# Kernel tuning notes

Hardware: AMD Instinct MI355X
Metric: run time of the kernel (lower is better)

Reference implementation:

```python
import jax, jax.numpy as jnp
import numpy as np

B, NV, NQ = 32, 256, 512
VD, QD, HD, K, HOUT = 512, 512, 512, 3, 8
HK = HD * K
BN_EPS = 1e-5


def _wn_linear(x, V, g, b):
    # weight_norm with dim=None: w = g * V / ||V||_F (scalar g)
    w = V * (g / jnp.linalg.norm(V))
    return x @ w.T + b


def setup_inputs() -> dict:
    key = jax.random.key(0)
    ks = jax.random.split(key, 12)
    n = lambda i, shape, s=1.0: jax.random.normal(ks[i], shape, jnp.float32) * s
    return {
        "v": n(0, (B, NV, VD)),
        "q": n(1, (B, NQ, QD)),
        # v_net / q_net: single weight-normed Linear + ReLU (dropout is eval-identity)
        "v_V": n(2, (HK, VD), 0.02),
        "v_g": jnp.float32(12.0),
        "v_b": n(3, (HK,), 0.02),
        "q_V": n(4, (HK, QD), 0.02),
        "q_g": jnp.float32(12.0),
        "q_b": n(5, (HK,), 0.02),
        "h_mat": n(6, (1, HOUT, 1, HK)),
        "h_bias": n(7, (1, HOUT, 1, 1)),
        "bn_gamma": jnp.ones((HD,), jnp.float32),
        "bn_beta": jnp.zeros((HD,), jnp.float32),
    }


def reference(v, q, v_V, v_g, v_b, q_V, q_g, q_b, h_mat, h_bias, bn_gamma, bn_beta):
    # projected features: (B, NV, HK) and (B, NQ, HK)
    v_ = jax.nn.relu(_wn_linear(v, v_V, v_g, v_b))
    q_ = jax.nn.relu(_wn_linear(q, q_V, q_g, q_b))
    # bilinear attention maps: (B, HOUT, NV, NQ)
    att_maps = jnp.einsum('hk,bvk,bqk->bhvq', h_mat[0, :, 0, :], v_, q_) + h_bias
    # fused version of the per-head loop: sum over heads h of einsum('bvk,bvq,bqk->bk')
    fusion = jnp.einsum('bvk,bhvq,bqk->bk', v_, att_maps, q_)  # (B, HK)
    # AvgPool1d(k, stride=k) * k == sum over contiguous groups of k
    logits = fusion.reshape(B, HD, K).sum(-1)
    # BatchNorm1d with batch statistics (train-mode math, biased variance)
    mu = logits.mean(axis=0)
    var = jnp.mean((logits - mu) ** 2, axis=0)
    logits = (logits - mu) * jax.lax.rsqrt(var + BN_EPS) * bn_gamma + bn_beta
    return logits, att_maps
```

## Files before the change

kernel.cpp:

```cpp
#include <hip/hip_runtime.h>
#include <hip/hip_bf16.h>

typedef unsigned short u16;
typedef unsigned int   u32;

typedef __attribute__((ext_vector_type(8))) short bhalf8;
typedef __attribute__((ext_vector_type(4))) float floatx4;

#define DEVI __device__ __forceinline__

DEVI float b2f(u16 x) { return __uint_as_float(((u32)x) << 16); }
DEVI u16 f2b(float f) {
    u32 u = __float_as_uint(f);
    u32 r = u + 0x7fffu + ((u >> 16) & 1u);
    return (u16)(r >> 16);
}
DEVI u32 pack2(float lo, float hi) {
    __hip_bfloat162 t = __float22bfloat162_rn(float2{lo, hi});
    union { __hip_bfloat162 b; u32 u; } c; c.b = t; return c.u;
}
DEVI u32 bmul2f(u32 a, u32 h) {
    float al = __uint_as_float(a << 16);
    float ah = __uint_as_float(a & 0xffff0000u);
    float hl = __uint_as_float(h << 16);
    float hh = __uint_as_float(h & 0xffff0000u);
    return pack2(al * hl, ah * hh);
}

DEVI void async16(const void* g, void* l) {
    __builtin_amdgcn_global_load_lds(
        (const __attribute__((address_space(1))) u32*)g,
        (__attribute__((address_space(3))) u32*)l, 16, 0, 0);
}

DEVI uint4 ld8(const void* p, size_t ei, int f32) {
    if (f32) {
        const float* f = (const float*)p + ei;
        float4 a = *(const float4*)f;
        float4 b = *(const float4*)(f + 4);
        uint4 r;
        r.x = pack2(a.x, a.y);
        r.y = pack2(a.z, a.w);
        r.z = pack2(b.x, b.y);
        r.w = pack2(b.z, b.w);
        return r;
    }
    return *(const uint4*)((const u16*)p + ei);
}
DEVI float ld1(const void* p, size_t ei, int f32) {
    return f32 ? ((const float*)p)[ei] : b2f(((const u16*)p)[ei]);
}
DEVI void st1(void* p, size_t ei, float v, int f32) {
    if (f32) ((float*)p)[ei] = v;
    else     ((u16*)p)[ei] = f2b(v);
}

__global__ void detect_kernel(const u32* __restrict__ bng, const u32* __restrict__ vg,
                              int* __restrict__ flags) {
    if (threadIdx.x == 0 && blockIdx.x == 0) {
        flags[0] = (bng[0] == 0x3F800000u) ? 1 : 0;
        flags[1] = (vg[0]  == 0x41400000u) ? 1 : 0;
    }
}

__global__ void convert_kernel(const void* __restrict__ src, u16* __restrict__ dst,
                               int n8, float* __restrict__ ssq,
                               const int* __restrict__ flags) {
    const int fa = flags[0];
    int i = blockIdx.x * 256 + threadIdx.x;
    const int stride = gridDim.x * 256;
    float s = 0.f;
    for (int c = i; c < n8; c += stride) {
        uint4 x = ld8(src, (size_t)c * 8, fa);
        *(uint4*)(dst + (size_t)c * 8) = x;
        if (ssq) {
            u32 a[4] = {x.x, x.y, x.z, x.w};
#pragma unroll
            for (int j = 0; j < 4; ++j) {
                float l = b2f((u16)a[j]), h = b2f((u16)(a[j] >> 16));
                s += l * l + h * h;
            }
        }
    }
    if (ssq) {
#pragma unroll
        for (int off = 32; off; off >>= 1) s += __shfl_down(s, off);
        if ((threadIdx.x & 63) == 0) atomicAdd(ssq, s);
    }
}

__global__ void sumsq_kernel(const void* __restrict__ a, const void* __restrict__ b,
                             float* __restrict__ out, const int* __restrict__ flags) {
    const int fa = flags[0];
    const int tid = threadIdx.x;
    int gid = blockIdx.x * 256 + tid;
    const int stride = gridDim.x * 256;
    float s0 = 0.f, s1 = 0.f;
    for (int c = gid; c < 786432 / 8; c += stride) {
        uint4 x = ld8(a, (size_t)c * 8, fa);
        uint4 y = ld8(b, (size_t)c * 8, fa);
        u32 ax[4] = {x.x, x.y, x.z, x.w};
        u32 ay[4] = {y.x, y.y, y.z, y.w};
#pragma unroll
        for (int i = 0; i < 4; ++i) {
            float l0 = b2f((u16)ax[i]), h0 = b2f((u16)(ax[i] >> 16));
            s0 += l0 * l0 + h0 * h0;
            float l1 = b2f((u16)ay[i]), h1 = b2f((u16)(ay[i] >> 16));
            s1 += l1 * l1 + h1 * h1;
        }
    }
#pragma unroll
    for (int off = 32; off; off >>= 1) {
        s0 += __shfl_down(s0, off);
        s1 += __shfl_down(s1, off);
    }
    if ((tid & 63) == 0) { atomicAdd(&out[0], s0); atomicAdd(&out[1], s1); }
}

DEVI bhalf8 fragLd(const u16* T, int row, int kb) {
    return *(const bhalf8*)&T[(row * 8 + (kb ^ (row & 7))) * 8];
}

__global__ __launch_bounds__(256, 2)
void proj_fast(const u16* __restrict__ X, const u16* __restrict__ V,
               const void* __restrict__ bias, const void* __restrict__ g,
               const float* __restrict__ sumsq, int sumsqIdx,
               u16* __restrict__ out, const int* __restrict__ flags) {
    const int fa = flags[0], fs = flags[1];
    const int tid = threadIdx.x, lane = tid & 63, w = tid >> 6;
    const int quad = lane >> 4, l15 = lane & 15;
    const int mBase = blockIdx.y * 128, nBase = blockIdx.x * 128;
    const int moff = (w & 1) * 64, noff = (w >> 1) * 64;
    __shared__ __align__(16) u16 As[128 * 64];
    __shared__ __align__(16) u16 Bs[128 * 64];
    floatx4 acc[4][4];
#pragma unroll
    for (int mi = 0; mi < 4; ++mi)
#pragma unroll
        for (int ni = 0; ni < 4; ++ni) acc[mi][ni] = floatx4{0.f, 0.f, 0.f, 0.f};

    for (int k0 = 0; k0 < 512; k0 += 64) {
#pragma unroll
        for (int r = 0; r < 4; ++r) {
            int s = r * 256 + tid;
            int row = s >> 3;
            int kb = (s & 7) ^ (row & 7);
            async16(X + (size_t)(mBase + row) * 512 + k0 + kb * 8,
                    As + (size_t)(r * 256 + w * 64) * 8);
            async16(V + (size_t)(nBase + row) * 512 + k0 + kb * 8,
                    Bs + (size_t)(r * 256 + w * 64) * 8);
        }
        __syncthreads();
#pragma unroll
        for (int ks = 0; ks < 64; ks += 32) {
            bhalf8 af[4], bfr[4];
#pragma unroll
            for (int i = 0; i < 4; ++i)
                af[i] = fragLd(As, moff + i * 16 + l15, (ks >> 3) + quad);
#pragma unroll
            for (int i = 0; i < 4; ++i)
                bfr[i] = fragLd(Bs, noff + i * 16 + l15, (ks >> 3) + quad);
#pragma unroll
            for (int mi = 0; mi < 4; ++mi)
#pragma unroll
                for (int ni = 0; ni < 4; ++ni)
                    acc[mi][ni] = __builtin_amdgcn_mfma_f32_16x16x32_bf16(
                        af[mi], bfr[ni], acc[mi][ni], 0, 0, 0);
        }
        __syncthreads();
    }
    const float scale = ld1(g, 0, fs) / sqrtf(sumsq[sumsqIdx]);
#pragma unroll
    for (int ni = 0; ni < 4; ++ni) {
        const int col = nBase + noff + ni * 16 + l15;
        const float bv = ld1(bias, col, fa);
#pragma unroll
        for (int mi = 0; mi < 4; ++mi) {
            const int rowb = mBase + moff + mi * 16 + quad * 4;
#pragma unroll
            for (int r = 0; r < 4; ++r) {
                float vv = acc[mi][ni][r] * scale + bv;
                vv = vv > 0.f ? vv : 0.f;
                out[(size_t)(rowb + r) * 1536 + col] = f2b(vv);
            }
        }
    }
}

__global__ __launch_bounds__(256, 2)
void proj_slow(const void* __restrict__ X, const void* __restrict__ V,
               const void* __restrict__ bias, const void* __restrict__ g,
               const float* __restrict__ sumsq, int sumsqIdx,
               u16* __restrict__ out, const int* __restrict__ flags) {
    const int fa = flags[0], fs = flags[1];
    const int tid = threadIdx.x, lane = tid & 63, w = tid >> 6;
    const int quad = lane >> 4, l15 = lane & 15;
    const int mBase = blockIdx.y * 128, nBase = blockIdx.x * 128;
    const int moff = (w & 1) * 64, noff = (w >> 1) * 64;
    __shared__ __align__(16) u16 As[128 * 64];
    __shared__ __align__(16) u16 Bs[128 * 64];
    floatx4 acc[4][4];
#pragma unroll
    for (int mi = 0; mi < 4; ++mi)
#pragma unroll
        for (int ni = 0; ni < 4; ++ni) acc[mi][ni] = floatx4{0.f, 0.f, 0.f, 0.f};

    for (int k0 = 0; k0 < 512; k0 += 64) {
        uint4 xa[4], xb[4];
#pragma unroll
        for (int r = 0; r < 4; ++r) {
            int s = r * 256 + tid;
            int row = s >> 3, kb = (s & 7) ^ (row & 7);
            xa[r] = ld8(X, (size_t)(mBase + row) * 512 + k0 + kb * 8, fa);
            xb[r] = ld8(V, (size_t)(nBase + row) * 512 + k0 + kb * 8, fa);
        }
#pragma unroll
        for (int r = 0; r < 4; ++r) {
            int s = r * 256 + tid;
            *(uint4*)&As[s * 8] = xa[r];
            *(uint4*)&Bs[s * 8] = xb[r];
        }
        __syncthreads();
#pragma unroll
        for (int ks = 0; ks < 64; ks += 32) {
            bhalf8 af[4], bfr[4];
#pragma unroll
            for (int i = 0; i < 4; ++i)
                af[i] = fragLd(As, moff + i * 16 + l15, (ks >> 3) + quad);
#pragma unroll
            for (int i = 0; i < 4; ++i)
                bfr[i] = fragLd(Bs, noff + i * 16 + l15, (ks >> 3) + quad);
#pragma unroll
            for (int mi = 0; mi < 4; ++mi)
#pragma unroll
                for (int ni = 0; ni < 4; ++ni)
                    acc[mi][ni] = __builtin_amdgcn_mfma_f32_16x16x32_bf16(
                        af[mi], bfr[ni], acc[mi][ni], 0, 0, 0);
        }
        __syncthreads();
    }
    const float scale = ld1(g, 0, fs) / sqrtf(sumsq[sumsqIdx]);
#pragma unroll
    for (int ni = 0; ni < 4; ++ni) {
        const int col = nBase + noff + ni * 16 + l15;
        const float bv = ld1(bias, col, fa);
#pragma unroll
        for (int mi = 0; mi < 4; ++mi) {
            const int rowb = mBase + moff + mi * 16 + quad * 4;
#pragma unroll
            for (int r = 0; r < 4; ++r) {
                float vv = acc[mi][ni][r] * scale + bv;
                vv = vv > 0.f ? vv : 0.f;
                out[(size_t)(rowb + r) * 1536 + col] = f2b(vv);
            }
        }
    }
}

__global__ __launch_bounds__(256, 2)
void att_kernel(const u16* __restrict__ v_, const u16* __restrict__ q_,
                const void* __restrict__ hmat, const void* __restrict__ hbias,
                void* __restrict__ dout, u16* __restrict__ sOut,
                const int* __restrict__ flags) {
    const int fa = flags[0];
    const int b = blockIdx.z, h = blockIdx.y;
    const int mt = blockIdx.x;
    const int tid = threadIdx.x, lane = tid & 63, w = tid >> 6;
    const int quad = lane >> 4, l15 = lane & 15;
    const int noff = w * 128;
    __shared__ __align__(16) u16 As[64 * 64];
    __shared__ __align__(16) u16 Bs[512 * 64];
    __shared__ __align__(16) u16 Hs[1536];
    const u16* vp = v_ + (size_t)b * 256 * 1536;
    const u16* qp = q_ + (size_t)b * 512 * 1536;

    if (h < 8) {
        if (tid < 192) *(uint4*)&Hs[tid * 8] = ld8(hmat, (size_t)h * 1536 + tid * 8, fa);
    } else {
        for (int k = tid; k < 1536; k += 256) {
            float s = 0.f;
#pragma unroll
            for (int hh = 0; hh < 8; ++hh) s += ld1(hmat, (size_t)hh * 1536 + k, fa);
            Hs[k] = f2b(s);
        }
    }
    __syncthreads();

    floatx4 acc[4][8];
#pragma unroll
    for (int mi = 0; mi < 4; ++mi)
#pragma unroll
        for (int ni = 0; ni < 8; ++ni) acc[mi][ni] = floatx4{0.f, 0.f, 0.f, 0.f};

    for (int k0 = 0; k0 < 1536; k0 += 64) {
#pragma unroll
        for (int r = 0; r < 16; ++r) {
            int s = r * 256 + tid;
            int row = s >> 3, kb = (s & 7) ^ (row & 7);
            async16(qp + (size_t)row * 1536 + k0 + kb * 8,
                    Bs + (size_t)(r * 256 + w * 64) * 8);
        }
#pragma unroll
        for (int r = 0; r < 2; ++r) {
            int s = r * 256 + tid;
            int row = s >> 3, kb = (s & 7) ^ (row & 7);
            uint4 a = *(const uint4*)(vp + (size_t)(mt * 64 + row) * 1536 + k0 + kb * 8);
            uint4 hh = *(const uint4*)&Hs[k0 + kb * 8];
            uint4 res;
            res.x = bmul2f(a.x, hh.x); res.y = bmul2f(a.y, hh.y);
            res.z = bmul2f(a.z, hh.z); res.w = bmul2f(a.w, hh.w);
            *(uint4*)&As[s * 8] = res;
        }
        __syncthreads();
#pragma unroll
        for (int ks = 0; ks < 64; ks += 32) {
            bhalf8 af[4], bfr[8];
#pragma unroll
            for (int i = 0; i < 4; ++i)
                af[i] = fragLd(As, i * 16 + l15, (ks >> 3) + quad);
#pragma unroll
            for (int i = 0; i < 8; ++i)
                bfr[i] = fragLd(Bs, noff + i * 16 + l15, (ks >> 3) + quad);
#pragma unroll
            for (int mi = 0; mi < 4; ++mi)
#pragma unroll
                for (int ni = 0; ni < 8; ++ni)
                    acc[mi][ni] = __builtin_amdgcn_mfma_f32_16x16x32_bf16(
                        af[mi], bfr[ni], acc[mi][ni], 0, 0, 0);
        }
        __syncthreads();
    }

    if (h < 8) {
        const float bias = ld1(hbias, h, fa);
        const size_t obase = 16384 + ((size_t)(b * 8 + h)) * 256 * 512;
#pragma unroll
        for (int mi = 0; mi < 4; ++mi) {
            const int vg = mt * 64 + mi * 16 + quad * 4;
#pragma unroll
            for (int ni = 0; ni < 8; ++ni) {
                const int qg = noff + ni * 16 + l15;
#pragma unroll
                for (int r = 0; r < 4; ++r)
                    st1(dout, obase + (size_t)(vg + r) * 512 + qg,
                        acc[mi][ni][r] + bias, fa);
            }
        }
    } else {
        float sbias = 0.f;
#pragma unroll
        for (int hh = 0; hh < 8; ++hh) sbias += ld1(hbias, hh, fa);
        u16* sp = sOut + (size_t)b * 256 * 512;
#pragma unroll
        for (int mi = 0; mi < 4; ++mi) {
            const int vg = mt * 64 + mi * 16 + quad * 4;
#pragma unroll
            for (int ni = 0; ni < 8; ++ni) {
                const int qg = noff + ni * 16 + l15;
#pragma unroll
                for (int r = 0; r < 4; ++r)
                    sp[(size_t)(vg + r) * 512 + qg] = f2b(acc[mi][ni][r] + sbias);
            }
        }
    }
}

__global__ __launch_bounds__(256, 2)
void fusion_kernel(const u16* __restrict__ s, const u16* __restrict__ q_,
                   const u16* __restrict__ v_, float* __restrict__ fusion) {
    const int b = blockIdx.y;
    const int vt = blockIdx.x / 12, kt = blockIdx.x % 12;
    const int tid = threadIdx.x, lane = tid & 63, w = tid >> 6;
    const int quad = lane >> 4, l15 = lane & 15;
    const int moff = (w & 1) * 64, noff = (w >> 1) * 64;
    __shared__ __align__(16) u16 As[128 * 64];
    __shared__ __align__(16) u16 Bs[128 * 64];
    const u16* ap = s + (size_t)b * 256 * 512;
    const u16* qp = q_ + (size_t)b * 512 * 1536;
    floatx4 acc[4][4];
#pragma unroll
    for (int mi = 0; mi < 4; ++mi)
#pragma unroll
        for (int ni = 0; ni < 4; ++ni) acc[mi][ni] = floatx4{0.f, 0.f, 0.f, 0.f};

    for (int q0 = 0; q0 < 512; q0 += 64) {
#pragma unroll
        for (int r = 0; r < 4; ++r) {
            int sl = r * 256 + tid;
            int row = sl >> 3, kb = (sl & 7) ^ (row & 7);
            async16(ap + (size_t)(vt * 128 + row) * 512 + q0 + kb * 8,
                    As + (size_t)(r * 256 + w * 64) * 8);
        }
        union { uint4 q4; u16 e[8]; } pk[4];
#pragma unroll
        for (int r = 0; r < 4; ++r) {
            int chunk = r * 256 + tid;
            int qq = chunk >> 4, n8 = chunk & 15;
            pk[r].q4 = *(const uint4*)(qp + (size_t)(q0 + qq) * 1536 + kt * 128 + n8 * 8);
        }
#pragma unroll
        for (int r = 0; r < 4; ++r) {
            int chunk = r * 256 + tid;
            int qq = chunk >> 4, n8 = chunk & 15;
            const int qs = qq ^ ((n8 & 7) << 3);
#pragma unroll
            for (int j = 0; j < 8; ++j)
                Bs[(n8 * 8 + j) * 64 + qs] = pk[r].e[j];
        }
        __syncthreads();
#pragma unroll
        for (int ks = 0; ks < 64; ks += 32) {
            bhalf8 af[4], bfr[4];
#pragma unroll
            for (int i = 0; i < 4; ++i)
                af[i] = fragLd(As, moff + i * 16 + l15, (ks >> 3) + quad);
#pragma unroll
            for (int i = 0; i < 4; ++i) {
                const int n = noff + i * 16 + l15;
                const int blk = ((ks >> 3) + quad) ^ ((n >> 3) & 7);
                bfr[i] = *(const bhalf8*)&Bs[n * 64 + (blk << 3)];
            }
#pragma unroll
            for (int mi = 0; mi < 4; ++mi)
#pragma unroll
                for (int ni = 0; ni < 4; ++ni)
                    acc[mi][ni] = __builtin_amdgcn_mfma_f32_16x16x32_bf16(
                        af[mi], bfr[ni], acc[mi][ni], 0, 0, 0);
        }
        __syncthreads();
    }
    const u16* vb = v_ + (size_t)b * 256 * 1536;
#pragma unroll
    for (int ni = 0; ni < 4; ++ni) {
        const int kg = kt * 128 + noff + ni * 16 + l15;
        float cs = 0.f;
#pragma unroll
        for (int mi = 0; mi < 4; ++mi) {
            const int vg = vt * 128 + moff + mi * 16 + quad * 4;
#pragma unroll
            for (int r = 0; r < 4; ++r)
                cs += acc[mi][ni][r] * b2f(vb[(size_t)(vg + r) * 1536 + kg]);
        }
        cs += __shfl_xor(cs, 16);
        cs += __shfl_xor(cs, 32);
        if (quad == 0) atomicAdd(&fusion[b * 1536 + kg], cs);
    }
}

__global__ void logits_kernel(const float* __restrict__ fusion, const void* __restrict__ gamma,
                              const void* __restrict__ beta, void* __restrict__ dout,
                              const int* __restrict__ flags) {
    const int fa = flags[0];
    const int d = blockIdx.x * 64 + threadIdx.x;
    float g[32];
    float mu = 0.f;
#pragma unroll
    for (int b = 0; b < 32; ++b) {
        const float* f = fusion + b * 1536 + d * 3;
        g[b] = f[0] + f[1] + f[2];
        mu += g[b];
    }
    mu *= (1.f / 32.f);
    float var = 0.f;
#pragma unroll
    for (int b = 0; b < 32; ++b) { float t = g[b] - mu; var += t * t; }
    var *= (1.f / 32.f);
    const float rs = rsqrtf(var + 1e-5f);
    const float ga = ld1(gamma, d, fa), be = ld1(beta, d, fa);
#pragma unroll
    for (int b = 0; b < 32; ++b)
        st1(dout, (size_t)b * 512 + d, (g[b] - mu) * rs * ga + be, fa);
}

extern "C" void kernel_launch(void* const* d_in, const int* in_sizes, int n_in,
                              void* d_out, int out_size, void* d_ws, size_t ws_size,
                              hipStream_t stream) {
    const void* v   = d_in[0];
    const void* q   = d_in[1];
    const void* vV  = d_in[2];
    const void* vg  = d_in[3];
    const void* vb  = d_in[4];
    const void* qV  = d_in[5];
    const void* qg  = d_in[6];
    const void* qb  = d_in[7];
    const void* hm  = d_in[8];
    const void* hb  = d_in[9];
    const void* bng = d_in[10];
    const void* bnb = d_in[11];

    char* ws = (char*)d_ws;
    float* sums   = (float*)ws;
    int*   flags  = (int*)(ws + 64);
    float* fusion = (float*)(ws + 256);

    const size_t NEED = 104006144;
    const bool fast = (ws_size >= NEED);

    hipMemsetAsync(sums, 0, 8, stream);
    hipMemsetAsync(fusion, 0, 32 * 1536 * 4, stream);
    detect_kernel<<<dim3(1), dim3(64), 0, stream>>>((const u32*)bng, (const u32*)vg, flags);

    if (fast) {
        u16* sbuf = (u16*)(ws + 197120);
        u16* vbf  = (u16*)(ws + 197120);
        u16* vVbf = (u16*)(ws + 8585728);
        u16* qVbf = (u16*)(ws + 10158592);
        u16* v_   = (u16*)(ws + 11731456);
        u16* q_   = (u16*)(ws + 36897280);
        u16* qbf  = (u16*)(ws + 87228928);

        convert_kernel<<<dim3(512), dim3(256), 0, stream>>>(v,  vbf,  524288, nullptr, flags);
        convert_kernel<<<dim3(1024), dim3(256), 0, stream>>>(q, qbf, 1048576, nullptr, flags);
        convert_kernel<<<dim3(128), dim3(256), 0, stream>>>(vV, vVbf, 98304, sums + 0, flags);
        convert_kernel<<<dim3(128), dim3(256), 0, stream>>>(qV, qVbf, 98304, sums + 1, flags);

        proj_fast<<<dim3(12, 64), dim3(256), 0, stream>>>(vbf, vVbf, vb, vg, sums, 0, v_, flags);
        proj_fast<<<dim3(12, 128), dim3(256), 0, stream>>>(qbf, qVbf, qb, qg, sums, 1, q_, flags);
        att_kernel<<<dim3(4, 9, 32), dim3(256), 0, stream>>>(v_, q_, hm, hb, d_out, sbuf, flags);
        fusion_kernel<<<dim3(24, 32), dim3(256), 0, stream>>>(sbuf, q_, v_, fusion);
    } else {
        u16* sbuf = (u16*)(ws + 197120);
        u16* v_   = (u16*)(ws + 8585728);
        u16* q_   = (u16*)(ws + 33751552);

        sumsq_kernel<<<dim3(128), dim3(256), 0, stream>>>(vV, qV, sums, flags);
        proj_slow<<<dim3(12, 64), dim3(256), 0, stream>>>(v, vV, vb, vg, sums, 0, v_, flags);
        proj_slow<<<dim3(12, 128), dim3(256), 0, stream>>>(q, qV, qb, qg, sums, 1, q_, flags);
        att_kernel<<<dim3(4, 9, 32), dim3(256), 0, stream>>>(v_, q_, hm, hb, d_out, sbuf, flags);
        fusion_kernel<<<dim3(24, 32), dim3(256), 0, stream>>>(sbuf, q_, v_, fusion);
    }
    logits_kernel<<<dim3(8), dim3(64), 0, stream>>>(fusion, bng, bnb, d_out, flags);
}
```

Before: 462.4 us.

## Compute all heads per attention tile with double-buffered fp16 MFMA

The attention kernel is restructured so each 512-thread block handles a 64x128 (v,q) tile for all 8 heads at once. It reuses the same v/q fragments across heads by scaling the v fragment with each head's row in registers, and forms the head-summed map from the per-head accumulators. This replaces the old 9-block-per-tile scheme that reloaded q_ for every head plus a separate summed-head pass. Loads are double-buffered with async global-to-LDS copies, blocks are remapped with a swizzled 1D grid, and intermediates switch from bf16 to fp16 MFMA. The fp16 switch risks overflow or precision differences, and 64 fp32 accumulators plus a larger LDS footprint may limit occupancy.

```diff
diff --git a/kernel.cpp b/kernel.cpp
--- a/kernel.cpp
+++ b/kernel.cpp
@@ -1,10 +1,11 @@
 #include <hip/hip_runtime.h>
 #include <hip/hip_bf16.h>
+#include <hip/hip_fp16.h>
 
 typedef unsigned short u16;
 typedef unsigned int   u32;
 
-typedef __attribute__((ext_vector_type(8))) short bhalf8;
+typedef __attribute__((ext_vector_type(8))) _Float16 half8;
 typedef __attribute__((ext_vector_type(4))) float floatx4;
 
 #define DEVI __device__ __forceinline__
@@ -15,16 +16,16 @@
     u32 r = u + 0x7fffu + ((u >> 16) & 1u);
     return (u16)(r >> 16);
 }
-DEVI u32 pack2(float lo, float hi) {
-    __hip_bfloat162 t = __float22bfloat162_rn(float2{lo, hi});
-    union { __hip_bfloat162 b; u32 u; } c; c.b = t; return c.u;
-}
-DEVI u32 bmul2f(u32 a, u32 h) {
-    float al = __uint_as_float(a << 16);
-    float ah = __uint_as_float(a & 0xffff0000u);
-    float hl = __uint_as_float(h << 16);
-    float hh = __uint_as_float(h & 0xffff0000u);
-    return pack2(al * hl, ah * hh);
+DEVI u16 f2h(float f) {
+    union { _Float16 h; u16 u; } c; c.h = (_Float16)f; return c.u;
+}
+DEVI float h2f(u16 x) {
+    union { u16 u; _Float16 h; } c; c.u = x; return (float)c.h;
+}
+DEVI u32 packh2(float lo, float hi) {
+    union { __half2 h; u32 u; } c;
+    c.h = __floats2half2_rn(lo, hi);
+    return c.u;
 }
 
 DEVI void async16(const void* g, void* l) {
@@ -33,19 +34,24 @@
         (__attribute__((address_space(3))) u32*)l, 16, 0, 0);
 }
 
-DEVI uint4 ld8(const void* p, size_t ei, int f32) {
+DEVI uint4 ld8h(const void* p, size_t ei, int f32) {
+    uint4 r;
     if (f32) {
         const float* f = (const float*)p + ei;
         float4 a = *(const float4*)f;
         float4 b = *(const float4*)(f + 4);
-        uint4 r;
-        r.x = pack2(a.x, a.y);
-        r.y = pack2(a.z, a.w);
-        r.z = pack2(b.x, b.y);
-        r.w = pack2(b.z, b.w);
-        return r;
-    }
-    return *(const uint4*)((const u16*)p + ei);
+        r.x = packh2(a.x, a.y);
+        r.y = packh2(a.z, a.w);
+        r.z = packh2(b.x, b.y);
+        r.w = packh2(b.z, b.w);
+    } else {
+        uint4 x = *(const uint4*)((const u16*)p + ei);
+        r.x = packh2(b2f((u16)x.x), b2f((u16)(x.x >> 16)));
+        r.y = packh2(b2f((u16)x.y), b2f((u16)(x.y >> 16)));
+        r.z = packh2(b2f((u16)x.z), b2f((u16)(x.z >> 16)));
+        r.w = packh2(b2f((u16)x.w), b2f((u16)(x.w >> 16)));
+    }
+    return r;
 }
 DEVI float ld1(const void* p, size_t ei, int f32) {
     return f32 ? ((const float*)p)[ei] : b2f(((const u16*)p)[ei]);
@@ -53,6 +59,10 @@
 DEVI void st1(void* p, size_t ei, float v, int f32) {
     if (f32) ((float*)p)[ei] = v;
     else     ((u16*)p)[ei] = f2b(v);
+}
+
+DEVI floatx4 mfma16(half8 a, half8 b, floatx4 c) {
+    return __builtin_amdgcn_mfma_f32_16x16x32_f16(a, b, c, 0, 0, 0);
 }
 
 __global__ void detect_kernel(const u32* __restrict__ bng, const u32* __restrict__ vg,
@@ -71,13 +81,13 @@
     const int stride = gridDim.x * 256;
     float s = 0.f;
     for (int c = i; c < n8; c += stride) {
-        uint4 x = ld8(src, (size_t)c * 8, fa);
+        uint4 x = ld8h(src, (size_t)c * 8, fa);
         *(uint4*)(dst + (size_t)c * 8) = x;
         if (ssq) {
             u32 a[4] = {x.x, x.y, x.z, x.w};
 #pragma unroll
             for (int j = 0; j < 4; ++j) {
-                float l = b2f((u16)a[j]), h = b2f((u16)(a[j] >> 16));
+                float l = h2f((u16)a[j]), h = h2f((u16)(a[j] >> 16));
                 s += l * l + h * h;
             }
         }
@@ -97,15 +107,15 @@
     const int stride = gridDim.x * 256;
     float s0 = 0.f, s1 = 0.f;
     for (int c = gid; c < 786432 / 8; c += stride) {
-        uint4 x = ld8(a, (size_t)c * 8, fa);
-        uint4 y = ld8(b, (size_t)c * 8, fa);
+        uint4 x = ld8h(a, (size_t)c * 8, fa);
+        uint4 y = ld8h(b, (size_t)c * 8, fa);
         u32 ax[4] = {x.x, x.y, x.z, x.w};
         u32 ay[4] = {y.x, y.y, y.z, y.w};
 #pragma unroll
         for (int i = 0; i < 4; ++i) {
-            float l0 = b2f((u16)ax[i]), h0 = b2f((u16)(ax[i] >> 16));
+            float l0 = h2f((u16)ax[i]), h0 = h2f((u16)(ax[i] >> 16));
             s0 += l0 * l0 + h0 * h0;
-            float l1 = b2f((u16)ay[i]), h1 = b2f((u16)(ay[i] >> 16));
+            float l1 = h2f((u16)ay[i]), h1 = h2f((u16)(ay[i] >> 16));
             s1 += l1 * l1 + h1 * h1;
         }
     }
@@ -117,8 +127,8 @@
     if ((tid & 63) == 0) { atomicAdd(&out[0], s0); atomicAdd(&out[1], s1); }
 }
 
-DEVI bhalf8 fragLd(const u16* T, int row, int kb) {
-    return *(const bhalf8*)&T[(row * 8 + (kb ^ (row & 7))) * 8];
+DEVI half8 fragLd(const u16* T, int row, int kb) {
+    return *(const half8*)&T[(row * 8 + (kb ^ (row & 7))) * 8];
 }
 
 __global__ __launch_bounds__(256, 2)
@@ -153,7 +163,7 @@
         __syncthreads();
 #pragma unroll
         for (int ks = 0; ks < 64; ks += 32) {
-            bhalf8 af[4], bfr[4];
+            half8 af[4], bfr[4];
 #pragma unroll
             for (int i = 0; i < 4; ++i)
                 af[i] = fragLd(As, moff + i * 16 + l15, (ks >> 3) + quad);
@@ -164,8 +174,7 @@
             for (int mi = 0; mi < 4; ++mi)
 #pragma unroll
                 for (int ni = 0; ni < 4; ++ni)
-                    acc[mi][ni] = __builtin_amdgcn_mfma_f32_16x16x32_bf16(
-                        af[mi], bfr[ni], acc[mi][ni], 0, 0, 0);
+                    acc[mi][ni] = mfma16(af[mi], bfr[ni], acc[mi][ni]);
         }
         __syncthreads();
     }
@@ -181,7 +190,7 @@
             for (int r = 0; r < 4; ++r) {
                 float vv = acc[mi][ni][r] * scale + bv;
                 vv = vv > 0.f ? vv : 0.f;
-                out[(size_t)(rowb + r) * 1536 + col] = f2b(vv);
+                out[(size_t)(rowb + r) * 1536 + col] = f2h(vv);
             }
         }
     }
@@ -211,8 +220,8 @@
         for (int r = 0; r < 4; ++r) {
             int s = r * 256 + tid;
             int row = s >> 3, kb = (s & 7) ^ (row & 7);
-            xa[r] = ld8(X, (size_t)(mBase + row) * 512 + k0 + kb * 8, fa);
-            xb[r] = ld8(V, (size_t)(nBase + row) * 512 + k0 + kb * 8, fa);
+            xa[r] = ld8h(X, (size_t)(mBase + row) * 512 + k0 + kb * 8, fa);
+            xb[r] = ld8h(V, (size_t)(nBase + row) * 512 + k0 + kb * 8, fa);
         }
 #pragma unroll
         for (int r = 0; r < 4; ++r) {
@@ -223,7 +232,7 @@
         __syncthreads();
 #pragma unroll
         for (int ks = 0; ks < 64; ks += 32) {
-            bhalf8 af[4], bfr[4];
+            half8 af[4], bfr[4];
 #pragma unroll
             for (int i = 0; i < 4; ++i)
                 af[i] = fragLd(As, moff + i * 16 + l15, (ks >> 3) + quad);
@@ -234,8 +243,7 @@
             for (int mi = 0; mi < 4; ++mi)
 #pragma unroll
                 for (int ni = 0; ni < 4; ++ni)
-                    acc[mi][ni] = __builtin_amdgcn_mfma_f32_16x16x32_bf16(
-                        af[mi], bfr[ni], acc[mi][ni], 0, 0, 0);
+                    acc[mi][ni] = mfma16(af[mi], bfr[ni], acc[mi][ni]);
         }
         __syncthreads();
     }
@@ -251,115 +259,127 @@
             for (int r = 0; r < 4; ++r) {
                 float vv = acc[mi][ni][r] * scale + bv;
                 vv = vv > 0.f ? vv : 0.f;
-                out[(size_t)(rowb + r) * 1536 + col] = f2b(vv);
-            }
-        }
-    }
-}
-
-__global__ __launch_bounds__(256, 2)
+                out[(size_t)(rowb + r) * 1536 + col] = f2h(vv);
+            }
+        }
+    }
+}
+
+__global__ __launch_bounds__(512, 2)
 void att_kernel(const u16* __restrict__ v_, const u16* __restrict__ q_,
                 const void* __restrict__ hmat, const void* __restrict__ hbias,
                 void* __restrict__ dout, u16* __restrict__ sOut,
                 const int* __restrict__ flags) {
     const int fa = flags[0];
-    const int b = blockIdx.z, h = blockIdx.y;
-    const int mt = blockIdx.x;
+    const int phys = blockIdx.x;
+    const int logical = (phys & 7) * 64 + (phys >> 3);
+    const int b = logical >> 4;
+    const int mt = (logical >> 2) & 3;
+    const int nt = logical & 3;
     const int tid = threadIdx.x, lane = tid & 63, w = tid >> 6;
     const int quad = lane >> 4, l15 = lane & 15;
-    const int noff = w * 128;
-    __shared__ __align__(16) u16 As[64 * 64];
-    __shared__ __align__(16) u16 Bs[512 * 64];
-    __shared__ __align__(16) u16 Hs[1536];
-    const u16* vp = v_ + (size_t)b * 256 * 1536;
-    const u16* qp = q_ + (size_t)b * 512 * 1536;
-
-    if (h < 8) {
-        if (tid < 192) *(uint4*)&Hs[tid * 8] = ld8(hmat, (size_t)h * 1536 + tid * 8, fa);
-    } else {
-        for (int k = tid; k < 1536; k += 256) {
-            float s = 0.f;
-#pragma unroll
-            for (int hh = 0; hh < 8; ++hh) s += ld1(hmat, (size_t)hh * 1536 + k, fa);
-            Hs[k] = f2b(s);
-        }
-    }
+    const int wr = (w >> 2) * 32;
+    const int wc = (w & 3) * 32;
+
+    __shared__ __align__(16) u16 Af[2][64 * 64];
+    __shared__ __align__(16) u16 Bf[2][128 * 64];
+    __shared__ __align__(16) u16 Hs[8 * 1536];
+
+    const u16* vp = v_ + (size_t)b * 256 * 1536 + (size_t)mt * 64 * 1536;
+    const u16* qp = q_ + (size_t)b * 512 * 1536 + (size_t)nt * 128 * 1536;
+
+#pragma unroll
+    for (int r = 0; r < 3; ++r) {
+        int slot = r * 512 + tid;
+        *(uint4*)&Hs[slot * 8] = ld8h(hmat, (size_t)slot * 8, fa);
+    }
+
+    auto STAGE = [&](int pbuf, int k0s) {
+        int s = tid;
+        int row = s >> 3, kb = (s & 7) ^ (row & 7);
+        async16(vp + (size_t)row * 1536 + k0s + kb * 8, &Af[pbuf][(w * 64) * 8]);
+#pragma unroll
+        for (int r = 0; r < 2; ++r) {
+            int s2 = r * 512 + tid;
+            int row2 = s2 >> 3, kb2 = (s2 & 7) ^ (row2 & 7);
+            async16(qp + (size_t)row2 * 1536 + k0s + kb2 * 8,
+                    &Bf[pbuf][(r * 512 + w * 64) * 8]);
+        }
+    };
+
+    STAGE(0, 0);
     __syncthreads();
 
-    floatx4 acc[4][8];
-#pragma unroll
-    for (int mi = 0; mi < 4; ++mi)
-#pragma unroll
-        for (int ni = 0; ni < 8; ++ni) acc[mi][ni] = floatx4{0.f, 0.f, 0.f, 0.f};
-
-    for (int k0 = 0; k0 < 1536; k0 += 64) {
-#pragma unroll
-        for (int r = 0; r < 16; ++r) {
-            int s = r * 256 + tid;
-            int row = s >> 3, kb = (s & 7) ^ (row & 7);
-            async16(qp + (size_t)row * 1536 + k0 + kb * 8,
-                    Bs + (size_t)(r * 256 + w * 64) * 8);
-        }
-#pragma unroll
-        for (int r = 0; r < 2; ++r) {
-            int s = r * 256 + tid;
-            int row = s >> 3, kb = (s & 7) ^ (row & 7);
-            uint4 a = *(const uint4*)(vp + (size_t)(mt * 64 + row) * 1536 + k0 + kb * 8);
-            uint4 hh = *(const uint4*)&Hs[k0 + kb * 8];
-            uint4 res;
-            res.x = bmul2f(a.x, hh.x); res.y = bmul2f(a.y, hh.y);
-            res.z = bmul2f(a.z, hh.z); res.w = bmul2f(a.w, hh.w);
-            *(uint4*)&As[s * 8] = res;
-        }
-        __syncthreads();
-#pragma unroll
-        for (int ks = 0; ks < 64; ks += 32) {
-            bhalf8 af[4], bfr[8];
-#pragma unroll
-            for (int i = 0; i < 4; ++i)
-                af[i] = fragLd(As, i * 16 + l15, (ks >> 3) + quad);
-#pragma unroll
-            for (int i = 0; i < 8; ++i)
-                bfr[i] = fragLd(Bs, noff + i * 16 + l15, (ks >> 3) + quad);
-#pragma unroll
-            for (int mi = 0; mi < 4; ++mi)
-#pragma unroll
-                for (int ni = 0; ni < 8; ++ni)
-                    acc[mi][ni] = __builtin_amdgcn_mfma_f32_16x16x32_bf16(
-                        af[mi], bfr[ni], acc[mi][ni], 0, 0, 0);
-        }
-        __syncthreads();
-    }
-
-    if (h < 8) {
-        const float bias = ld1(hbias, h, fa);
+    floatx4 acc[8][2][2];
+#pragma unroll
+    for (int h = 0; h < 8; ++h)
+#pragma unroll
+        for (int mi = 0; mi < 2; ++mi)
+#pragma unroll
+            for (int ni = 0; ni < 2; ++ni) acc[h][mi][ni] = floatx4{0.f, 0.f, 0.f, 0.f};
+
+    int pb = 0;
+    for (int kt = 0; kt < 24; ++kt) {
+        const int k0 = kt * 64;
+        if (kt < 23) STAGE(pb ^ 1, k0 + 64);
+        const u16* As = Af[pb];
+        const u16* Bs = Bf[pb];
+#pragma unroll
+        for (int ks = 0; ks < 2; ++ks) {
+            const int ch = ks * 4 + quad;
+            half8 av0 = fragLd(As, wr + l15, ch);
+            half8 av1 = fragLd(As, wr + 16 + l15, ch);
+            half8 bq0 = fragLd(Bs, wc + l15, ch);
+            half8 bq1 = fragLd(Bs, wc + 16 + l15, ch);
+#pragma unroll
+            for (int h = 0; h < 8; ++h) {
+                half8 hf = *(const half8*)&Hs[h * 1536 + k0 + ch * 8];
+                half8 a0 = av0 * hf;
+                half8 a1 = av1 * hf;
+                acc[h][0][0] = mfma16(a0, bq0, acc[h][0][0]);
+                acc[h][0][1] = mfma16(a0, bq1, acc[h][0][1]);
+                acc[h][1][0] = mfma16(a1, bq0, acc[h][1][0]);
+                acc[h][1][1] = mfma16(a1, bq1, acc[h][1][1]);
+            }
+        }
+        __syncthreads();
+        pb ^= 1;
+    }
+
+    float hb8[8];
+    float sbias = 0.f;
+#pragma unroll
+    for (int h = 0; h < 8; ++h) { hb8[h] = ld1(hbias, h, fa); sbias += hb8[h]; }
+
+#pragma unroll
+    for (int h = 0; h < 8; ++h) {
         const size_t obase = 16384 + ((size_t)(b * 8 + h)) * 256 * 512;
 #pragma unroll
-        for (int mi = 0; mi < 4; ++mi) {
-            const int vg = mt * 64 + mi * 16 + quad * 4;
-#pragma unroll
-            for (int ni = 0; ni < 8; ++ni) {
-                const int qg = noff + ni * 16 + l15;
+        for (int mi = 0; mi < 2; ++mi) {
+            const int vg = mt * 64 + wr + mi * 16 + quad * 4;
+#pragma unroll
+            for (int ni = 0; ni < 2; ++ni) {
+                const int qg = nt * 128 + wc + ni * 16 + l15;
 #pragma unroll
                 for (int r = 0; r < 4; ++r)
                     st1(dout, obase + (size_t)(vg + r) * 512 + qg,
-                        acc[mi][ni][r] + bias, fa);
-            }
-        }
-    } else {
-        float sbias = 0.f;
-#pragma unroll
-        for (int hh = 0; hh < 8; ++hh) sbias += ld1(hbias, hh, fa);
-        u16* sp = sOut + (size_t)b * 256 * 512;
-#pragma unroll
-        for (int mi = 0; mi < 4; ++mi) {
-            const int vg = mt * 64 + mi * 16 + quad * 4;
-#pragma unroll
-            for (int ni = 0; ni < 8; ++ni) {
-                const int qg = noff + ni * 16 + l15;
-#pragma unroll
-                for (int r = 0; r < 4; ++r)
-                    sp[(size_t)(vg + r) * 512 + qg] = f2b(acc[mi][ni][r] + sbias);
+                        acc[h][mi][ni][r] + hb8[h], fa);
+            }
+        }
+    }
+    u16* sp = sOut + (size_t)b * 256 * 512;
+#pragma unroll
+    for (int mi = 0; mi < 2; ++mi) {
+        const int vg = mt * 64 + wr + mi * 16 + quad * 4;
+#pragma unroll
+        for (int ni = 0; ni < 2; ++ni) {
+            const int qg = nt * 128 + wc + ni * 16 + l15;
+#pragma unroll
+            for (int r = 0; r < 4; ++r) {
+                float s = sbias;
+#pragma unroll
+                for (int h = 0; h < 8; ++h) s += acc[h][mi][ni][r];
+                sp[(size_t)(vg + r) * 512 + qg] = f2h(s);
             }
         }
     }
@@ -410,7 +430,7 @@
         __syncthreads();
 #pragma unroll
         for (int ks = 0; ks < 64; ks += 32) {
-            bhalf8 af[4], bfr[4];
+            half8 af[4], bfr[4];
 #pragma unroll
             for (int i = 0; i < 4; ++i)
                 af[i] = fragLd(As, moff + i * 16 + l15, (ks >> 3) + quad);
@@ -418,14 +438,13 @@
             for (int i = 0; i < 4; ++i) {
                 const int n = noff + i * 16 + l15;
                 const int blk = ((ks >> 3) + quad) ^ ((n >> 3) & 7);
-                bfr[i] = *(const bhalf8*)&Bs[n * 64 + (blk << 3)];
+                bfr[i] = *(const half8*)&Bs[n * 64 + (blk << 3)];
             }
 #pragma unroll
             for (int mi = 0; mi < 4; ++mi)
 #pragma unroll
                 for (int ni = 0; ni < 4; ++ni)
-                    acc[mi][ni] = __builtin_amdgcn_mfma_f32_16x16x32_bf16(
-                        af[mi], bfr[ni], acc[mi][ni], 0, 0, 0);
+                    acc[mi][ni] = mfma16(af[mi], bfr[ni], acc[mi][ni]);
         }
         __syncthreads();
     }
@@ -439,7 +458,7 @@
             const int vg = vt * 128 + moff + mi * 16 + quad * 4;
 #pragma unroll
             for (int r = 0; r < 4; ++r)
-                cs += acc[mi][ni][r] * b2f(vb[(size_t)(vg + r) * 1536 + kg]);
+                cs += acc[mi][ni][r] * h2f(vb[(size_t)(vg + r) * 1536 + kg]);
         }
         cs += __shfl_xor(cs, 16);
         cs += __shfl_xor(cs, 32);
@@ -516,7 +535,7 @@
 
         proj_fast<<<dim3(12, 64), dim3(256), 0, stream>>>(vbf, vVbf, vb, vg, sums, 0, v_, flags);
         proj_fast<<<dim3(12, 128), dim3(256), 0, stream>>>(qbf, qVbf, qb, qg, sums, 1, q_, flags);
-        att_kernel<<<dim3(4, 9, 32), dim3(256), 0, stream>>>(v_, q_, hm, hb, d_out, sbuf, flags);
+        att_kernel<<<dim3(512), dim3(512), 0, stream>>>(v_, q_, hm, hb, d_out, sbuf, flags);
         fusion_kernel<<<dim3(24, 32), dim3(256), 0, stream>>>(sbuf, q_, v_, fusion);
     } else {
         u16* sbuf = (u16*)(ws + 197120);
@@ -526,7 +545,7 @@
         sumsq_kernel<<<dim3(128), dim3(256), 0, stream>>>(vV, qV, sums, flags);
         proj_slow<<<dim3(12, 64), dim3(256), 0, stream>>>(v, vV, vb, vg, sums, 0, v_, flags);
         proj_slow<<<dim3(12, 128), dim3(256), 0, stream>>>(q, qV, qb, qg, sums, 1, q_, flags);
-        att_kernel<<<dim3(4, 9, 32), dim3(256), 0, stream>>>(v_, q_, hm, hb, d_out, sbuf, flags);
+        att_kernel<<<dim3(512), dim3(512), 0, stream>>>(v_, q_, hm, hb, d_out, sbuf, flags);
         fusion_kernel<<<dim3(24, 32), dim3(256), 0, stream>>>(sbuf, q_, v_, fusion);
     }
     logits_kernel<<<dim3(8), dim3(64), 0, stream>>>(fusion, bng, bnb, d_out, flags);
```

Measured after the change: 439.0 us. 5.1% less time.
